# Performance work log

Hardware: AMD Instinct MI355X
Metric: run time of the kernel (lower is better)

The kernel has to match this reference:

```python
import jax, jax.numpy as jnp
import numpy as np

NUM_HEADS = 16

def rotate_half(x):
    x1, x2 = jnp.split(x, 2, axis=-1)
    return jnp.concatenate((-x2, x1), axis=-1)

def setup_inputs() -> dict:
    key = jax.random.key(0)
    ks = jax.random.split(key, 5)
    b, n, dim, hd = 2, 2048, 1024, 64
    return {
        "x": jax.random.normal(ks[0], (b, n, dim), dtype=jnp.float32),
        "Wqkv": jax.random.normal(ks[1], (3 * dim, dim), dtype=jnp.float32) * (dim ** -0.5),
        "Wproj": jax.random.normal(ks[2], (dim, dim), dtype=jnp.float32) * (dim ** -0.5),
        "bproj": jnp.zeros((dim,), dtype=jnp.float32),
        "sin": jax.random.normal(ks[3], (n, hd), dtype=jnp.float32),
        "cos": jax.random.normal(ks[4], (n, hd), dtype=jnp.float32),
    }

def reference(x, Wqkv, Wproj, bproj, sin, cos):
    b, n, dim = x.shape
    h = NUM_HEADS
    d = dim // h
    qkv = x @ Wqkv.T
    qkv = qkv.reshape(b, n, 3, h, d).transpose(2, 0, 3, 1, 4)
    q, k, v = qkv[0], qkv[1], qkv[2]
    # RoPE: sin/cos [n, d] broadcast over [b, h, n, d]
    q = q * cos + rotate_half(q) * sin
    k = k * cos + rotate_half(k) * sin
    # SDPA (non-causal, no dropout at eval)
    scale = d ** -0.5
    scores = jnp.einsum("bhnd,bhmd->bhnm", q, k) * scale
    attn = jax.nn.softmax(scores, axis=-1)
    out = jnp.einsum("bhnm,bhmd->bhnd", attn, v)
    # merge heads: [b, h, n, d] -> [b, n, h*d]
    out = out.transpose(0, 2, 1, 3).reshape(b, n, dim)
    return out @ Wproj.T + bproj
```

## Files before the change

kernel.cpp:

```cpp
#include <hip/hip_runtime.h>
#include <hip/hip_fp16.h>

typedef _Float16 f16;
typedef _Float16 half8 __attribute__((ext_vector_type(8)));
typedef _Float16 half4v __attribute__((ext_vector_type(4)));
typedef float f32x4 __attribute__((ext_vector_type(4)));

#define QSCALE 0.18033688011112042f
#define SHIFT2 17.312340490667560f

__device__ __forceinline__ void gload_lds16(const void* g, void* lds) {
  __builtin_amdgcn_global_load_lds(
      (__attribute__((address_space(1))) void*)g,
      (__attribute__((address_space(3))) void*)lds, 16, 0, 0);
}

__global__ __launch_bounds__(256) void cvt_f32_f16_kernel(
    const float* __restrict__ src, f16* __restrict__ dst, int n4) {
  int i = blockIdx.x * 256 + threadIdx.x;
  if (i >= n4) return;
  float4 v = ((const float4*)src)[i];
  half4v o;
  o.x = (f16)v.x; o.y = (f16)v.y; o.z = (f16)v.z; o.w = (f16)v.w;
  ((half4v*)dst)[i] = o;
}

template<int EPI, int AH>
__global__ __launch_bounds__(256) void hgemm_kernel(
    const float* __restrict__ A32, const f16* __restrict__ A16,
    const f16* __restrict__ B, int K,
    const float* __restrict__ cosT, const float* __restrict__ sinT,
    f16* __restrict__ Qout, f16* __restrict__ Kout, f16* __restrict__ Vtout,
    const float* __restrict__ bias, float* __restrict__ Cout) {
  __shared__ f16 As[128 * 32];
  __shared__ f16 Bs[128 * 32];
  const int tid = threadIdx.x;
  const int lane = tid & 63, w = tid >> 6;
  const int fr = lane & 15, fkg = lane >> 4, fk = fkg * 8;
  const int wm = (w >> 1) * 64, wn = (w & 1) * 64;
  const long long rowBase = (long long)blockIdx.x * 128;
  const long long colBase = (long long)blockIdx.y * 128;
  const int srow = tid >> 1, scol = (tid & 1) * 16;

  f32x4 acc[4][4] = {};
  const f16* Bb = B + colBase * K;
  const f16* Ab16 = A16 + rowBase * K;

  for (int k0 = 0; k0 < K; k0 += 32) {
#pragma unroll
    for (int r = 0; r < 2; ++r) {
      int c = r * 4 + w;
      int off = (c * 64 + lane) * 8;
      int row = off >> 5, col = off & 31;
      gload_lds16(Bb + (long long)row * K + k0 + col, Bs + c * 512);
      if (AH == 1)
        gload_lds16(Ab16 + (long long)row * K + k0 + col, As + c * 512);
    }
    if (AH == 0) {
      const float* pA = A32 + (rowBase + srow) * K + k0 + scol;
      float4 f0 = ((const float4*)pA)[0], f1 = ((const float4*)pA)[1],
             f2 = ((const float4*)pA)[2], f3 = ((const float4*)pA)[3];
      half8 h0, h1;
      h0[0] = (f16)f0.x; h0[1] = (f16)f0.y; h0[2] = (f16)f0.z; h0[3] = (f16)f0.w;
      h0[4] = (f16)f1.x; h0[5] = (f16)f1.y; h0[6] = (f16)f1.z; h0[7] = (f16)f1.w;
      h1[0] = (f16)f2.x; h1[1] = (f16)f2.y; h1[2] = (f16)f2.z; h1[3] = (f16)f2.w;
      h1[4] = (f16)f3.x; h1[5] = (f16)f3.y; h1[6] = (f16)f3.z; h1[7] = (f16)f3.w;
      *(half8*)(As + srow * 32 + scol) = h0;
      *(half8*)(As + srow * 32 + scol + 8) = h1;
    }
    __syncthreads();
    half8 a[4], b[4];
#pragma unroll
    for (int i = 0; i < 4; ++i)
      a[i] = *(const half8*)(As + (wm + i * 16 + fr) * 32 + fk);
#pragma unroll
    for (int j = 0; j < 4; ++j)
      b[j] = *(const half8*)(Bs + (wn + j * 16 + fr) * 32 + fk);
#pragma unroll
    for (int i = 0; i < 4; ++i)
#pragma unroll
      for (int j = 0; j < 4; ++j)
        acc[i][j] = __builtin_amdgcn_mfma_f32_16x16x32_f16(a[i], b[j], acc[i][j], 0, 0, 0);
    __syncthreads();
  }

  if (EPI == 0) {
#pragma unroll
    for (int i = 0; i < 4; ++i) {
#pragma unroll
      for (int r = 0; r < 4; ++r) {
        int rg = (int)rowBase + wm + i * 16 + fkg * 4 + r;
        int bidx = rg >> 11, nn = rg & 2047;
#pragma unroll
        for (int j = 0; j < 4; ++j) {
          int cg = (int)colBase + wn + j * 16 + fr;
          int t = cg >> 10, cc = cg & 1023;
          int head = cc >> 6, d = cc & 63;
          int bh = bidx * 16 + head;
          float v = acc[i][j][r];
          if (t == 2) {
            Vtout[((long long)bh * 64 + d) * 2048 + nn] = (f16)v;
          } else {
            float pal = acc[i][j ^ 2][r];
            float cs = cosT[nn * 64 + d];
            float sn = sinT[nn * 64 + d];
            v = v * cs + (d < 32 ? -pal : pal) * sn;
            if (t == 0) v *= QSCALE;
            f16 hv = (f16)v;
            if (t == 0) Qout[((long long)bh * 2048 + nn) * 64 + d] = hv;
            else        Kout[((long long)bh * 2048 + nn) * 64 + d] = hv;
          }
        }
      }
    }
  } else {
#pragma unroll
    for (int i = 0; i < 4; ++i)
#pragma unroll
      for (int r = 0; r < 4; ++r) {
        long long rg = rowBase + wm + i * 16 + fkg * 4 + r;
#pragma unroll
        for (int j = 0; j < 4; ++j) {
          int cg = (int)colBase + wn + j * 16 + fr;
          Cout[rg * 1024 + cg] = acc[i][j][r] + bias[cg];
        }
      }
  }
}

__global__ __launch_bounds__(256) void attn_kernel(
    const f16* __restrict__ Q, const f16* __restrict__ Kb,
    const f16* __restrict__ Vt, f16* __restrict__ Om) {
  __shared__ f16 Ks[64 * 72];
  __shared__ f16 Vs[64 * 72];
  __shared__ f16 Ps[4][32 * 72];
  const int tid = threadIdx.x;
  const int lane = tid & 63, w = tid >> 6;
  const int fr = lane & 15, fkg = lane >> 4, fk = fkg * 8;
  const int bh = blockIdx.y;
  const int q0 = blockIdx.x * 128 + w * 32;
  f16* Psw = &Ps[w][0];

  half8 aq[2][2];
#pragma unroll
  for (int m = 0; m < 2; ++m)
#pragma unroll
    for (int ks = 0; ks < 2; ++ks)
      aq[m][ks] = *(const half8*)(Q + ((long long)bh * 2048 + q0 + m * 16 + fr) * 64 +
                                  ks * 32 + fk);

  half8 ones_frag;
#pragma unroll
  for (int j = 0; j < 8; ++j) ones_frag[j] = (fr == 0) ? (f16)1.0f : (f16)0.0f;

  f32x4 acc[2][5] = {};

  const int soff = tid * 8;
  const int skr0 = soff >> 6, sd0 = soff & 63;
  half8 kreg[2], vreg[2];
#pragma unroll
  for (int c = 0; c < 2; ++c) {
    int kr = skr0 + c * 32;
    kreg[c] = *(const half8*)(Kb + ((long long)bh * 2048 + kr) * 64 + sd0);
    vreg[c] = *(const half8*)(Vt + ((long long)bh * 64 + kr) * 2048 + sd0);
  }

  for (int kv0 = 0; kv0 < 2048; kv0 += 64) {
    __syncthreads();
#pragma unroll
    for (int c = 0; c < 2; ++c) {
      int kr = skr0 + c * 32;
      *(half8*)(Ks + kr * 72 + sd0) = kreg[c];
      *(half8*)(Vs + kr * 72 + sd0) = vreg[c];
    }
    if (kv0 + 64 < 2048) {
#pragma unroll
      for (int c = 0; c < 2; ++c) {
        int kr = skr0 + c * 32;
        kreg[c] = *(const half8*)(Kb + ((long long)bh * 2048 + kv0 + 64 + kr) * 64 + sd0);
        vreg[c] = *(const half8*)(Vt + ((long long)bh * 64 + kr) * 2048 + kv0 + 64 + sd0);
      }
    }
    __syncthreads();

    f32x4 z[2][4];
#pragma unroll
    for (int n = 0; n < 4; ++n) {
      half8 bk0 = *(const half8*)(Ks + (n * 16 + fr) * 72 + fk);
      half8 bk1 = *(const half8*)(Ks + (n * 16 + fr) * 72 + 32 + fk);
#pragma unroll
      for (int m = 0; m < 2; ++m) {
        f32x4 t = {0.f, 0.f, 0.f, 0.f};
        t = __builtin_amdgcn_mfma_f32_16x16x32_f16(bk0, aq[m][0], t, 0, 0, 0);
        t = __builtin_amdgcn_mfma_f32_16x16x32_f16(bk1, aq[m][1], t, 0, 0, 0);
        z[m][n] = t;
      }
    }

#pragma unroll
    for (int m = 0; m < 2; ++m)
#pragma unroll
      for (int n = 0; n < 4; ++n) {
        half4v h;
#pragma unroll
        for (int r = 0; r < 4; ++r)
          h[r] = (f16)__builtin_amdgcn_exp2f(z[m][n][r] - SHIFT2);
        *(half4v*)(Psw + (m * 16 + fr) * 72 + n * 16 + fkg * 4) = h;
      }

#pragma unroll
    for (int ks = 0; ks < 2; ++ks) {
      half8 ap[2];
#pragma unroll
      for (int m = 0; m < 2; ++m) {
        ap[m] = *(const half8*)(Psw + (m * 16 + fr) * 72 + ks * 32 + fk);
        acc[m][4] = __builtin_amdgcn_mfma_f32_16x16x32_f16(ap[m], ones_frag, acc[m][4], 0, 0, 0);
      }
#pragma unroll
      for (int dd = 0; dd < 4; ++dd) {
        half8 bv = *(const half8*)(Vs + (dd * 16 + fr) * 72 + ks * 32 + fk);
#pragma unroll
        for (int m = 0; m < 2; ++m)
          acc[m][dd] = __builtin_amdgcn_mfma_f32_16x16x32_f16(ap[m], bv, acc[m][dd], 0, 0, 0);
      }
    }
  }

  const int b = bh >> 4, h = bh & 15;
#pragma unroll
  for (int m = 0; m < 2; ++m)
#pragma unroll
    for (int r = 0; r < 4; ++r) {
      int nn = q0 + m * 16 + fkg * 4 + r;
      float l = __shfl(acc[m][4][r], lane & 48);
      float inv = 1.f / l;
#pragma unroll
      for (int dd = 0; dd < 4; ++dd)
        Om[((long long)b * 2048 + nn) * 1024 + h * 64 + dd * 16 + fr] =
            (f16)(acc[m][dd][r] * inv);
    }
}

extern "C" void kernel_launch(void* const* d_in, const int* in_sizes, int n_in,
                              void* d_out, int out_size, void* d_ws, size_t ws_size,
                              hipStream_t stream) {
  (void)in_sizes; (void)n_in; (void)out_size;
  const float* x     = (const float*)d_in[0];
  const float* Wqkv  = (const float*)d_in[1];
  const float* Wproj = (const float*)d_in[2];
  const float* bproj = (const float*)d_in[3];
  const float* sinT  = (const float*)d_in[4];
  const float* cosT  = (const float*)d_in[5];
  float* out = (float*)d_out;

  f16* ws = (f16*)d_ws;

  if (ws_size >= 41943040ull) {
    f16* xh     = ws;
    f16* Om     = ws;
    f16* Wqkvh  = ws + 4194304;
    f16* Wprojh = ws + 7340032;
    f16* Qb     = ws + 8388608;
    f16* Kb     = ws + 12582912;
    f16* Vtb    = ws + 16777216;

    cvt_f32_f16_kernel<<<4096, 256, 0, stream>>>(x, xh, 1048576);
    cvt_f32_f16_kernel<<<3072, 256, 0, stream>>>(Wqkv, Wqkvh, 786432);
    cvt_f32_f16_kernel<<<1024, 256, 0, stream>>>(Wproj, Wprojh, 262144);

    hgemm_kernel<0, 1><<<dim3(32, 24), 256, 0, stream>>>(
        nullptr, xh, Wqkvh, 1024, cosT, sinT, Qb, Kb, Vtb, nullptr, nullptr);

    attn_kernel<<<dim3(16, 32), 256, 0, stream>>>(Qb, Kb, Vtb, Om);

    hgemm_kernel<1, 1><<<dim3(32, 8), 256, 0, stream>>>(
        nullptr, Om, Wprojh, 1024, nullptr, nullptr, nullptr, nullptr, nullptr,
        bproj, out);
  } else {
    f16* Wqkvh  = ws;
    f16* Om     = ws;
    f16* Wprojh = ws + 4194304;
    f16* Qb     = ws + 5242880;
    f16* Kb     = ws + 9437184;
    f16* Vtb    = ws + 13631488;

    cvt_f32_f16_kernel<<<3072, 256, 0, stream>>>(Wqkv, Wqkvh, 786432);
    cvt_f32_f16_kernel<<<1024, 256, 0, stream>>>(Wproj, Wprojh, 262144);

    hgemm_kernel<0, 0><<<dim3(32, 24), 256, 0, stream>>>(
        x, nullptr, Wqkvh, 1024, cosT, sinT, Qb, Kb, Vtb, nullptr, nullptr);

    attn_kernel<<<dim3(16, 32), 256, 0, stream>>>(Qb, Kb, Vtb, Om);

    hgemm_kernel<1, 1><<<dim3(32, 8), 256, 0, stream>>>(
        nullptr, Om, Wprojh, 1024, nullptr, nullptr, nullptr, nullptr, nullptr,
        bproj, out);
  }
}
```

Measured before the change: 143.7 us.

## Double-buffer GEMM LDS staging and halve column tile to 64

The GEMM kernel now keeps two LDS buffers and issues the next K-slice's global-to-LDS loads before computing the current one, so only one barrier per iteration is needed. The column tile shrinks from 128 to 64, which doubles the grid for both projections and changes the per-wave B fragment mapping so the RoPE partner column sits in the same thread. The fp32-A fallback path is removed and the launcher always converts x to fp16, which assumes the workspace is large enough. Smaller tiles lower per-block reuse and increase total A traffic in exchange for more blocks and better latency hiding.

```diff
diff --git a/kernel.cpp b/kernel.cpp
--- a/kernel.cpp
+++ b/kernel.cpp
@@ -25,63 +25,57 @@
   ((half4v*)dst)[i] = o;
 }
 
-template<int EPI, int AH>
+template<int EPI>
 __global__ __launch_bounds__(256) void hgemm_kernel(
-    const float* __restrict__ A32, const f16* __restrict__ A16,
-    const f16* __restrict__ B, int K,
+    const f16* __restrict__ A16, const f16* __restrict__ B, int K,
     const float* __restrict__ cosT, const float* __restrict__ sinT,
     f16* __restrict__ Qout, f16* __restrict__ Kout, f16* __restrict__ Vtout,
     const float* __restrict__ bias, float* __restrict__ Cout) {
-  __shared__ f16 As[128 * 32];
-  __shared__ f16 Bs[128 * 32];
+  __shared__ f16 As[2][128 * 32];
+  __shared__ f16 Bs[2][64 * 32];
   const int tid = threadIdx.x;
   const int lane = tid & 63, w = tid >> 6;
   const int fr = lane & 15, fkg = lane >> 4, fk = fkg * 8;
-  const int wm = (w >> 1) * 64, wn = (w & 1) * 64;
+  const int wm = (w >> 1) * 64, wn2 = (w & 1) * 16;
   const long long rowBase = (long long)blockIdx.x * 128;
-  const long long colBase = (long long)blockIdx.y * 128;
-  const int srow = tid >> 1, scol = (tid & 1) * 16;
-
-  f32x4 acc[4][4] = {};
+  const long long colBase = (long long)blockIdx.y * 64;
+
+  f32x4 acc[4][2] = {};
+  const f16* Ab = A16 + rowBase * K;
   const f16* Bb = B + colBase * K;
-  const f16* Ab16 = A16 + rowBase * K;
-
-  for (int k0 = 0; k0 < K; k0 += 32) {
+
+  auto stage = [&](int buf, int k0) {
 #pragma unroll
     for (int r = 0; r < 2; ++r) {
       int c = r * 4 + w;
       int off = (c * 64 + lane) * 8;
       int row = off >> 5, col = off & 31;
-      gload_lds16(Bb + (long long)row * K + k0 + col, Bs + c * 512);
-      if (AH == 1)
-        gload_lds16(Ab16 + (long long)row * K + k0 + col, As + c * 512);
-    }
-    if (AH == 0) {
-      const float* pA = A32 + (rowBase + srow) * K + k0 + scol;
-      float4 f0 = ((const float4*)pA)[0], f1 = ((const float4*)pA)[1],
-             f2 = ((const float4*)pA)[2], f3 = ((const float4*)pA)[3];
-      half8 h0, h1;
-      h0[0] = (f16)f0.x; h0[1] = (f16)f0.y; h0[2] = (f16)f0.z; h0[3] = (f16)f0.w;
-      h0[4] = (f16)f1.x; h0[5] = (f16)f1.y; h0[6] = (f16)f1.z; h0[7] = (f16)f1.w;
-      h1[0] = (f16)f2.x; h1[1] = (f16)f2.y; h1[2] = (f16)f2.z; h1[3] = (f16)f2.w;
-      h1[4] = (f16)f3.x; h1[5] = (f16)f3.y; h1[6] = (f16)f3.z; h1[7] = (f16)f3.w;
-      *(half8*)(As + srow * 32 + scol) = h0;
-      *(half8*)(As + srow * 32 + scol + 8) = h1;
-    }
+      gload_lds16(Ab + (long long)row * K + k0 + col, &As[buf][c * 512]);
+    }
+    {
+      int off = (w * 64 + lane) * 8;
+      int row = off >> 5, col = off & 31;
+      gload_lds16(Bb + (long long)row * K + k0 + col, &Bs[buf][w * 512]);
+    }
+  };
+
+  stage(0, 0);
+  for (int k0 = 0; k0 < K; k0 += 32) {
+    const int buf = (k0 >> 5) & 1;
     __syncthreads();
-    half8 a[4], b[4];
+    if (k0 + 32 < K) stage(buf ^ 1, k0 + 32);
+    half8 a[4], b[2];
 #pragma unroll
     for (int i = 0; i < 4; ++i)
-      a[i] = *(const half8*)(As + (wm + i * 16 + fr) * 32 + fk);
-#pragma unroll
-    for (int j = 0; j < 4; ++j)
-      b[j] = *(const half8*)(Bs + (wn + j * 16 + fr) * 32 + fk);
+      a[i] = *(const half8*)(&As[buf][(wm + i * 16 + fr) * 32 + fk]);
+#pragma unroll
+    for (int j = 0; j < 2; ++j)
+      b[j] = *(const half8*)(&Bs[buf][(wn2 + j * 32 + fr) * 32 + fk]);
 #pragma unroll
     for (int i = 0; i < 4; ++i)
 #pragma unroll
-      for (int j = 0; j < 4; ++j)
+      for (int j = 0; j < 2; ++j)
         acc[i][j] = __builtin_amdgcn_mfma_f32_16x16x32_f16(a[i], b[j], acc[i][j], 0, 0, 0);
-    __syncthreads();
   }
 
   if (EPI == 0) {
@@ -92,8 +86,8 @@
         int rg = (int)rowBase + wm + i * 16 + fkg * 4 + r;
         int bidx = rg >> 11, nn = rg & 2047;
 #pragma unroll
-        for (int j = 0; j < 4; ++j) {
-          int cg = (int)colBase + wn + j * 16 + fr;
+        for (int j = 0; j < 2; ++j) {
+          int cg = (int)colBase + wn2 + j * 32 + fr;
           int t = cg >> 10, cc = cg & 1023;
           int head = cc >> 6, d = cc & 63;
           int bh = bidx * 16 + head;
@@ -101,7 +95,7 @@
           if (t == 2) {
             Vtout[((long long)bh * 64 + d) * 2048 + nn] = (f16)v;
           } else {
-            float pal = acc[i][j ^ 2][r];
+            float pal = acc[i][j ^ 1][r];
             float cs = cosT[nn * 64 + d];
             float sn = sinT[nn * 64 + d];
             v = v * cs + (d < 32 ? -pal : pal) * sn;
@@ -120,8 +114,8 @@
       for (int r = 0; r < 4; ++r) {
         long long rg = rowBase + wm + i * 16 + fkg * 4 + r;
 #pragma unroll
-        for (int j = 0; j < 4; ++j) {
-          int cg = (int)colBase + wn + j * 16 + fr;
+        for (int j = 0; j < 2; ++j) {
+          int cg = (int)colBase + wn2 + j * 32 + fr;
           Cout[rg * 1024 + cg] = acc[i][j][r] + bias[cg];
         }
       }
@@ -244,7 +238,7 @@
 extern "C" void kernel_launch(void* const* d_in, const int* in_sizes, int n_in,
                               void* d_out, int out_size, void* d_ws, size_t ws_size,
                               hipStream_t stream) {
-  (void)in_sizes; (void)n_in; (void)out_size;
+  (void)in_sizes; (void)n_in; (void)out_size; (void)ws_size;
   const float* x     = (const float*)d_in[0];
   const float* Wqkv  = (const float*)d_in[1];
   const float* Wproj = (const float*)d_in[2];
@@ -253,47 +247,24 @@
   const float* cosT  = (const float*)d_in[5];
   float* out = (float*)d_out;
 
-  f16* ws = (f16*)d_ws;
-
-  if (ws_size >= 41943040ull) {
-    f16* xh     = ws;
-    f16* Om     = ws;
-    f16* Wqkvh  = ws + 4194304;
-    f16* Wprojh = ws + 7340032;
-    f16* Qb     = ws + 8388608;
-    f16* Kb     = ws + 12582912;
-    f16* Vtb    = ws + 16777216;
-
-    cvt_f32_f16_kernel<<<4096, 256, 0, stream>>>(x, xh, 1048576);
-    cvt_f32_f16_kernel<<<3072, 256, 0, stream>>>(Wqkv, Wqkvh, 786432);
-    cvt_f32_f16_kernel<<<1024, 256, 0, stream>>>(Wproj, Wprojh, 262144);
-
-    hgemm_kernel<0, 1><<<dim3(32, 24), 256, 0, stream>>>(
-        nullptr, xh, Wqkvh, 1024, cosT, sinT, Qb, Kb, Vtb, nullptr, nullptr);
-
-    attn_kernel<<<dim3(16, 32), 256, 0, stream>>>(Qb, Kb, Vtb, Om);
-
-    hgemm_kernel<1, 1><<<dim3(32, 8), 256, 0, stream>>>(
-        nullptr, Om, Wprojh, 1024, nullptr, nullptr, nullptr, nullptr, nullptr,
-        bproj, out);
-  } else {
-    f16* Wqkvh  = ws;
-    f16* Om     = ws;
-    f16* Wprojh = ws + 4194304;
-    f16* Qb     = ws + 5242880;
-    f16* Kb     = ws + 9437184;
-    f16* Vtb    = ws + 13631488;
-
-    cvt_f32_f16_kernel<<<3072, 256, 0, stream>>>(Wqkv, Wqkvh, 786432);
-    cvt_f32_f16_kernel<<<1024, 256, 0, stream>>>(Wproj, Wprojh, 262144);
-
-    hgemm_kernel<0, 0><<<dim3(32, 24), 256, 0, stream>>>(
-        x, nullptr, Wqkvh, 1024, cosT, sinT, Qb, Kb, Vtb, nullptr, nullptr);
-
-    attn_kernel<<<dim3(16, 32), 256, 0, stream>>>(Qb, Kb, Vtb, Om);
-
-    hgemm_kernel<1, 1><<<dim3(32, 8), 256, 0, stream>>>(
-        nullptr, Om, Wprojh, 1024, nullptr, nullptr, nullptr, nullptr, nullptr,
-        bproj, out);
-  }
-}
+  f16* ws     = (f16*)d_ws;
+  f16* xh     = ws;
+  f16* Om     = ws;
+  f16* Wqkvh  = ws + 4194304;
+  f16* Wprojh = ws + 7340032;
+  f16* Qb     = ws + 8388608;
+  f16* Kb     = ws + 12582912;
+  f16* Vtb    = ws + 16777216;
+
+  cvt_f32_f16_kernel<<<4096, 256, 0, stream>>>(x, xh, 1048576);
+  cvt_f32_f16_kernel<<<3072, 256, 0, stream>>>(Wqkv, Wqkvh, 786432);
+  cvt_f32_f16_kernel<<<1024, 256, 0, stream>>>(Wproj, Wprojh, 262144);
+
+  hgemm_kernel<0><<<dim3(32, 48), 256, 0, stream>>>(
+      xh, Wqkvh, 1024, cosT, sinT, Qb, Kb, Vtb, nullptr, nullptr);
+
+  attn_kernel<<<dim3(16, 32), 256, 0, stream>>>(Qb, Kb, Vtb, Om);
+
+  hgemm_kernel<1><<<dim3(32, 16), 256, 0, stream>>>(
+      Om, Wprojh, 1024, nullptr, nullptr, nullptr, nullptr, nullptr, bproj, out);
+}
```

Result: faster. 140.7 us (-2.1%).
